# Kernel optimization log

Hardware: AMD Instinct MI355X
Metric: run time of the kernel (lower is better)

## Reference

```python
import jax, jax.numpy as jnp
import numpy as np

B, T, D, H = 4, 2048, 1024, 16
HD = D // H  # head_dim = 64


def _make_freqs():
    # standard RoPE angles: theta_i = 10000^{-2i/hd}
    inv_freq = 1.0 / (10000.0 ** (np.arange(0, HD, 2, dtype=np.float32) / HD))  # [HD/2]
    angles = np.arange(T, dtype=np.float32)[:, None] * inv_freq[None, :]        # [T, HD/2]
    return jnp.asarray(np.cos(angles)), jnp.asarray(np.sin(angles))


def setup_inputs() -> dict:
    key = jax.random.key(0)
    ks = jax.random.split(key, 5)
    freqs_cos, freqs_sin = _make_freqs()
    s = 1.0 / np.sqrt(D)
    return {
        "q": jax.random.normal(ks[0], (B, T, D), jnp.float32),
        "freqs_cos": freqs_cos,
        "freqs_sin": freqs_sin,
        "qkv_w": jax.random.normal(ks[1], (3 * D, D), jnp.float32) * s,
        "qkv_b": jax.random.normal(ks[2], (3 * D,), jnp.float32) * 0.01,
        "o_w": jax.random.normal(ks[3], (D, D), jnp.float32) * s,
        "o_b": jax.random.normal(ks[4], (D,), jnp.float32) * 0.01,
    }


def _apply_rope(x, cos, sin):
    # x: [B, T, H, HD]; cos/sin: [T, HD/2]
    xr = x.reshape(*x.shape[:-1], HD // 2, 2)
    x0, x1 = xr[..., 0], xr[..., 1]
    c = cos[None, :, None, :]
    s = sin[None, :, None, :]
    o0 = x0 * c - x1 * s
    o1 = x0 * s + x1 * c
    return jnp.stack([o0, o1], axis=-1).reshape(x.shape)


def reference(q, freqs_cos, freqs_sin, qkv_w, qkv_b, o_w, o_b):
    # fused QKV projection (torch Linear: x @ W.T + b)
    qkv = q @ qkv_w.T + qkv_b                      # [B, T, 3D]
    qh, kh, vh = jnp.split(qkv, 3, axis=-1)
    qh = qh.reshape(B, T, H, HD)
    kh = kh.reshape(B, T, H, HD)
    vh = vh.reshape(B, T, H, HD)
    qh = _apply_rope(qh, freqs_cos, freqs_sin)
    kh = _apply_rope(kh, freqs_cos, freqs_sin)
    # scaled dot-product attention, no mask, no dropout (eval)
    scale = 1.0 / np.sqrt(HD)
    scores = jnp.einsum('bqhd,bkhd->bhqk', qh, kh) * scale
    probs = jax.nn.softmax(scores, axis=-1)
    out = jnp.einsum('bhqk,bkhd->bqhd', probs, vh).reshape(B, T, D)
    return out @ o_w.T + o_b
```

## Files before the change

### kernel.cpp

```cpp
#include <hip/hip_runtime.h>

#define B_  4
#define T_  2048
#define D_  1024
#define H_  16
#define HD_ 64
#define M_  8192
#define N1_ 3072
#define K_  1024

typedef __bf16 bf16x8 __attribute__((ext_vector_type(8)));
typedef float  f32x4  __attribute__((ext_vector_type(4)));
typedef float  f32x16 __attribute__((ext_vector_type(16)));

__device__ __forceinline__ unsigned short f2bf(float f) {
  union { float f; unsigned u; } v; v.f = f;
  unsigned u = v.u;
  unsigned r = (u + 0x7fffu + ((u >> 16) & 1u)) >> 16;
  return (unsigned short)r;
}
__device__ __forceinline__ float bf2f(unsigned short h) {
  union { unsigned u; float f; } v; v.u = ((unsigned)h) << 16;
  return v.f;
}
__device__ __forceinline__ unsigned pk2(float a, float b) {
  union { __bf16 h[2]; unsigned u; } t;
  t.h[0] = (__bf16)a; t.h[1] = (__bf16)b;
  return t.u;
}
__device__ __forceinline__ void plswap(unsigned &a, unsigned &b) {
  asm("v_permlane32_swap_b32 %0, %1" : "+v"(a), "+v"(b));
}
__device__ __forceinline__ float fexp2(float x) {
  float r;
  asm("v_exp_f32 %0, %1" : "=v"(r) : "v"(x));
  return r;
}

__device__ __forceinline__ void gl_lds16(const unsigned short* g, unsigned short* l) {
  __builtin_amdgcn_global_load_lds(
      (const __attribute__((address_space(1))) unsigned int*)g,
      (__attribute__((address_space(3))) unsigned int*)l,
      16, 0, 0);
}

#define NQ4  ((M_*K_)/4)
#define NW14 ((N1_*K_)/4)
#define NW24 ((D_*K_)/4)
__global__ void cvt_all(const float* __restrict__ q, const float* __restrict__ w1,
                        const float* __restrict__ w2,
                        unsigned short* __restrict__ qo, unsigned short* __restrict__ w1o,
                        unsigned short* __restrict__ w2o) {
  int i = blockIdx.x * 256 + threadIdx.x;
  const float* in; unsigned short* out; int idx;
  if (i < NQ4)              { in = q;  out = qo;  idx = i; }
  else if (i < NQ4 + NW14)  { in = w1; out = w1o; idx = i - NQ4; }
  else if (i < NQ4 + NW14 + NW24) { in = w2; out = w2o; idx = i - NQ4 - NW14; }
  else return;
  float4 f = ((const float4*)in)[idx];
  ushort4 o;
  o.x = f2bf(f.x); o.y = f2bf(f.y); o.z = f2bf(f.z); o.w = f2bf(f.w);
  ((ushort4*)out)[idx] = o;
}

__global__ __launch_bounds__(256) void gemm_qkv(
    const unsigned short* __restrict__ A,
    const unsigned short* __restrict__ W,
    const float* __restrict__ bias,
    unsigned short* __restrict__ Qg,
    unsigned short* __restrict__ Kg,
    unsigned short* __restrict__ Vt,
    const float* __restrict__ cosb, const float* __restrict__ sinb)
{
  __shared__ unsigned short As[128*64];
  __shared__ unsigned short Bs[128*64];
  const int tid = threadIdx.x;
  const int lane = tid & 63, wave = tid >> 6;
  const int wr = wave >> 1, wc = wave & 1;
  const int lr = lane & 15, lg = lane >> 4;
  const int sw = lr & 7;
  const long m0 = (long)blockIdx.x * 128;
  const int  n0 = blockIdx.y * 128;

  f32x4 acc[4][4];
#pragma unroll
  for (int i = 0; i < 4; ++i)
#pragma unroll
    for (int j = 0; j < 4; ++j) acc[i][j] = (f32x4){0.f,0.f,0.f,0.f};

  for (int kt = 0; kt < K_/64; ++kt) {
    __syncthreads();
#pragma unroll
    for (int p = 0; p < 4; ++p) {
      int slot = p*256 + tid;
      int row = slot >> 3, sc = slot & 7, ch = sc ^ (row & 7);
      gl_lds16(A + (m0 + row)*K_ + kt*64 + ch*8, &As[slot*8]);
      gl_lds16(W + ((long)n0 + row)*K_ + kt*64 + ch*8, &Bs[slot*8]);
    }
    __syncthreads();
#pragma unroll
    for (int kk = 0; kk < 2; ++kk) {
      bf16x8 af[4], bfr[4];
#pragma unroll
      for (int i = 0; i < 4; ++i) {
        af[i]  = *(const bf16x8*)&As[(wr*64 + i*16 + lr)*64 + (((lg + 4*kk) ^ sw) * 8)];
        bfr[i] = *(const bf16x8*)&Bs[(wc*64 + i*16 + lr)*64 + (((lg + 4*kk) ^ sw) * 8)];
      }
#pragma unroll
      for (int i = 0; i < 4; ++i)
#pragma unroll
        for (int j = 0; j < 4; ++j)
          acc[i][j] = __builtin_amdgcn_mfma_f32_16x16x32_bf16(af[i], bfr[j], acc[i][j], 0, 0, 0);
    }
  }

#pragma unroll
  for (int j = 0; j < 4; ++j) {
    int n = n0 + wc*64 + j*16 + lr;
    float bv = bias[n];
    int part = n >> 10;
    int d = n & 1023;
    int h = d >> 6, hd = d & 63;
    if (part == 2) {
#pragma unroll
      for (int i = 0; i < 4; ++i) {
        long m = m0 + wr*64 + i*16 + lg*4;
        int b = (int)(m >> 11), t = (int)(m & 2047);
        ushort4 st;
        st.x = f2bf(acc[i][j][0] + bv);
        st.y = f2bf(acc[i][j][1] + bv);
        st.z = f2bf(acc[i][j][2] + bv);
        st.w = f2bf(acc[i][j][3] + bv);
        *(ushort4*)(Vt + ((long)((b*H_ + h)*HD_ + hd))*T_ + t) = st;
      }
    } else if (part == 0) {
#pragma unroll
      for (int i = 0; i < 4; ++i) {
#pragma unroll
        for (int r = 0; r < 4; ++r) {
          long m = m0 + wr*64 + i*16 + lg*4 + r;
          int b = (int)(m >> 11), t = (int)(m & 2047);
          Qg[(((long)(b*H_ + h))*T_ + t)*HD_ + hd] = f2bf(acc[i][j][r] + bv);
        }
      }
    } else {
      const int u   = hd >> 1;
      const int odd = lr & 1;
#pragma unroll
      for (int i = 0; i < 4; ++i) {
#pragma unroll
        for (int r = 0; r < 4; ++r) {
          long m = m0 + wr*64 + i*16 + lg*4 + r;
          int b = (int)(m >> 11), t = (int)(m & 2047);
          float v = acc[i][j][r] + bv;
          float p = __shfl_xor(v, 1);
          float cu = cosb[t*32 + u], su = sinb[t*32 + u];
          float res = odd ? (p*su + v*cu) : (v*cu - p*su);
          Kg[(((long)(b*H_ + h))*T_ + t)*HD_ + hd] = f2bf(res);
        }
      }
    }
  }
}

__global__ __launch_bounds__(256) void flash_attn(
    const unsigned short* __restrict__ Qg, const unsigned short* __restrict__ Kg,
    const unsigned short* __restrict__ Vt, unsigned short* __restrict__ attn,
    const float* __restrict__ cosb, const float* __restrict__ sinb)
{
  __shared__ unsigned short Ks0[64*64], Vs0[64*64];
  __shared__ unsigned short Ks1[64*64], Vs1[64*64];
  const int tid = threadIdx.x, lane = tid & 63, wave = tid >> 6;
  const int lq = lane & 31, hi = lane >> 5;
  const int id = blockIdx.x;
  const int bh = (id & 7)*8 + ((id >> 3) & 7);
  const int q0 = (id >> 6)*128 + wave*32;
  const long kvbase = (long)bh * T_ * HD_;
  const int fsw = (lq & 7) ^ (lq >> 3);

  bf16x8 qf[4];
  {
    const int tq = q0 + lq;
    const unsigned short* qrow = Qg + kvbase + (long)tq*HD_;
    const float* crow = cosb + tq*32;
    const float* srow = sinb + tq*32;
    const float scl = 0.125f * 1.44269504f;
#pragma unroll
    for (int c = 0; c < 4; ++c) {
      bf16x8 raw = *(const bf16x8*)(qrow + c*16 + hi*8);
      const unsigned short* e = (const unsigned short*)&raw;
      bf16x8 outv;
#pragma unroll
      for (int j = 0; j < 4; ++j) {
        float x0 = bf2f(e[2*j]), x1 = bf2f(e[2*j+1]);
        float cv = crow[c*8 + hi*4 + j], sv = srow[c*8 + hi*4 + j];
        outv[2*j]   = (__bf16)((x0*cv - x1*sv) * scl);
        outv[2*j+1] = (__bf16)((x0*sv + x1*cv) * scl);
      }
      qf[c] = outv;
    }
  }

  f32x16 oA, oB;
#pragma unroll
  for (int r = 0; r < 16; ++r) { oA[r] = 0.f; oB[r] = 0.f; }
  float l = 0.f;

  const int slotA = tid, slotB = 256 + tid;
  const int rwA = slotA >> 3, rwB = slotB >> 3;
  const int chA = (slotA & 7) ^ ((rwA & 7) ^ ((rwA >> 3) & 7));
  const int chB = (slotB & 7) ^ ((rwB & 7) ^ ((rwB >> 3) & 7));
  const unsigned short* KsrcA = Kg + kvbase + (long)rwA*HD_ + chA*8;
  const unsigned short* KsrcB = Kg + kvbase + (long)rwB*HD_ + chB*8;
  const unsigned short* VsrcA = Vt + (long)(bh*HD_ + rwA)*T_ + chA*8;
  const unsigned short* VsrcB = Vt + (long)(bh*HD_ + rwB)*T_ + chB*8;

#define STAGE0(kt) {                                      \
    gl_lds16(KsrcA + (kt)*64*HD_, &Ks0[slotA*8]);         \
    gl_lds16(KsrcB + (kt)*64*HD_, &Ks0[slotB*8]);         \
    gl_lds16(VsrcA + (kt)*64,     &Vs0[slotA*8]);         \
    gl_lds16(VsrcB + (kt)*64,     &Vs0[slotB*8]);         \
  }
#define STAGE1(kt) {                                      \
    gl_lds16(KsrcA + (kt)*64*HD_, &Ks1[slotA*8]);         \
    gl_lds16(KsrcB + (kt)*64*HD_, &Ks1[slotB*8]);         \
    gl_lds16(VsrcA + (kt)*64,     &Vs1[slotA*8]);         \
    gl_lds16(VsrcB + (kt)*64,     &Vs1[slotB*8]);         \
  }

#define FBODY(KSB, VSB)                                                                   \
  _Pragma("unroll")                                                                       \
  for (int kf = 0; kf < 2; ++kf) {                                                        \
    bf16x8 ka[4];                                                                         \
    _Pragma("unroll")                                                                     \
    for (int c = 0; c < 4; ++c)                                                           \
      ka[c] = *(const bf16x8*)&KSB[(kf*32 + lq)*64 + (((2*c + hi) ^ fsw ^ (kf*4)) * 8)];  \
    f32x16 cf;                                                                            \
    _Pragma("unroll")                                                                     \
    for (int r = 0; r < 16; ++r) cf[r] = 0.f;                                             \
    __builtin_amdgcn_s_setprio(1);                                                        \
    cf = __builtin_amdgcn_mfma_f32_32x32x16_bf16(ka[0], qf[0], cf, 0, 0, 0);              \
    cf = __builtin_amdgcn_mfma_f32_32x32x16_bf16(ka[1], qf[1], cf, 0, 0, 0);              \
    cf = __builtin_amdgcn_mfma_f32_32x32x16_bf16(ka[2], qf[2], cf, 0, 0, 0);              \
    cf = __builtin_amdgcn_mfma_f32_32x32x16_bf16(ka[3], qf[3], cf, 0, 0, 0);              \
    __builtin_amdgcn_s_setprio(0);                                                        \
    float p[16];                                                                          \
    _Pragma("unroll")                                                                     \
    for (int r = 0; r < 16; ++r) p[r] = fexp2(cf[r]);                                     \
    {                                                                                     \
      float s01 = (p[0]+p[1]) + (p[2]+p[3]);                                              \
      float s23 = (p[4]+p[5]) + (p[6]+p[7]);                                              \
      float s45 = (p[8]+p[9]) + (p[10]+p[11]);                                            \
      float s67 = (p[12]+p[13]) + (p[14]+p[15]);                                          \
      l += (s01 + s23) + (s45 + s67);                                                     \
    }                                                                                     \
    unsigned qx0 = pk2(p[0],  p[1]),  qy0 = pk2(p[2],  p[3]);                             \
    unsigned qx1 = pk2(p[4],  p[5]),  qy1 = pk2(p[6],  p[7]);                             \
    unsigned qx2 = pk2(p[8],  p[9]),  qy2 = pk2(p[10], p[11]);                            \
    unsigned qx3 = pk2(p[12], p[13]), qy3 = pk2(p[14], p[15]);                            \
    plswap(qx0, qx1); plswap(qy0, qy1);                                                   \
    plswap(qx2, qx3); plswap(qy2, qy3);                                                   \
    union { unsigned w[4]; bf16x8 v; } u0, u1;                                            \
    u0.w[0] = qx0; u0.w[1] = qy0; u0.w[2] = qx1; u0.w[3] = qy1;                           \
    u1.w[0] = qx2; u1.w[1] = qy2; u1.w[2] = qx3; u1.w[3] = qy3;                           \
    bf16x8 pf0 = u0.v, pf1 = u1.v;                                                        \
    bf16x8 va00 = *(const bf16x8*)&VSB[(lq)*64      + (((4*kf + 0 + hi) ^ fsw) * 8)];     \
    bf16x8 va01 = *(const bf16x8*)&VSB[(lq)*64      + (((4*kf + 2 + hi) ^ fsw) * 8)];     \
    bf16x8 va10 = *(const bf16x8*)&VSB[(32 + lq)*64 + (((4*kf + 0 + hi) ^ fsw ^ 4) * 8)]; \
    bf16x8 va11 = *(const bf16x8*)&VSB[(32 + lq)*64 + (((4*kf + 2 + hi) ^ fsw ^ 4) * 8)]; \
    __builtin_amdgcn_s_setprio(1);                                                        \
    oA = __builtin_amdgcn_mfma_f32_32x32x16_bf16(va00, pf0, oA, 0, 0, 0);                 \
    oA = __builtin_amdgcn_mfma_f32_32x32x16_bf16(va01, pf1, oA, 0, 0, 0);                 \
    oB = __builtin_amdgcn_mfma_f32_32x32x16_bf16(va10, pf0, oB, 0, 0, 0);                 \
    oB = __builtin_amdgcn_mfma_f32_32x32x16_bf16(va11, pf1, oB, 0, 0, 0);                 \
    __builtin_amdgcn_s_setprio(0);                                                        \
  }

  STAGE0(0);
  __syncthreads();

  for (int kt = 0; kt < T_/64; kt += 2) {
    STAGE1(kt + 1);
    FBODY(Ks0, Vs0);
    __syncthreads();
    if (kt + 2 < T_/64) STAGE0(kt + 2);
    FBODY(Ks1, Vs1);
    __syncthreads();
  }
#undef STAGE0
#undef STAGE1
#undef FBODY

  l += __shfl_xor(l, 32);
  int b = bh >> 4, h = bh & 15;
  float inv = 1.0f / l;
  long rowb = ((long)(b*T_ + q0 + lq))*D_ + h*HD_;
#pragma unroll
  for (int g = 0; g < 4; ++g) {
    ushort4 st;
    st.x = f2bf(oA[4*g+0] * inv);
    st.y = f2bf(oA[4*g+1] * inv);
    st.z = f2bf(oA[4*g+2] * inv);
    st.w = f2bf(oA[4*g+3] * inv);
    *(ushort4*)(attn + rowb + 8*g + 4*hi) = st;
  }
#pragma unroll
  for (int g = 0; g < 4; ++g) {
    ushort4 st;
    st.x = f2bf(oB[4*g+0] * inv);
    st.y = f2bf(oB[4*g+1] * inv);
    st.z = f2bf(oB[4*g+2] * inv);
    st.w = f2bf(oB[4*g+3] * inv);
    *(ushort4*)(attn + rowb + 32 + 8*g + 4*hi) = st;
  }
}

__global__ __launch_bounds__(256) void gemm_out(
    const unsigned short* __restrict__ A,
    const unsigned short* __restrict__ W,
    const float* __restrict__ bias,
    float* __restrict__ C)
{
  __shared__ unsigned short As[128*64];
  __shared__ unsigned short Bs[128*64];
  const int tid = threadIdx.x;
  const int lane = tid & 63, wave = tid >> 6;
  const int wr = wave >> 1, wc = wave & 1;
  const int lr = lane & 15, lg = lane >> 4;
  const int sw = lr & 7;
  const long m0 = (long)blockIdx.x * 128;
  const int  n0 = blockIdx.y * 128;

  f32x4 acc[4][4];
#pragma unroll
  for (int i = 0; i < 4; ++i)
#pragma unroll
    for (int j = 0; j < 4; ++j) acc[i][j] = (f32x4){0.f,0.f,0.f,0.f};

  for (int kt = 0; kt < K_/64; ++kt) {
    __syncthreads();
#pragma unroll
    for (int p = 0; p < 4; ++p) {
      int slot = p*256 + tid;
      int row = slot >> 3, sc = slot & 7, ch = sc ^ (row & 7);
      gl_lds16(A + (m0 + row)*K_ + kt*64 + ch*8, &As[slot*8]);
      gl_lds16(W + ((long)n0 + row)*K_ + kt*64 + ch*8, &Bs[slot*8]);
    }
    __syncthreads();
#pragma unroll
    for (int kk = 0; kk < 2; ++kk) {
      bf16x8 af[4], bfr[4];
#pragma unroll
      for (int i = 0; i < 4; ++i) {
        af[i]  = *(const bf16x8*)&As[(wr*64 + i*16 + lr)*64 + (((lg + 4*kk) ^ sw) * 8)];
        bfr[i] = *(const bf16x8*)&Bs[(wc*64 + i*16 + lr)*64 + (((lg + 4*kk) ^ sw) * 8)];
      }
#pragma unroll
      for (int i = 0; i < 4; ++i)
#pragma unroll
        for (int j = 0; j < 4; ++j)
          acc[i][j] = __builtin_amdgcn_mfma_f32_16x16x32_bf16(af[i], bfr[j], acc[i][j], 0, 0, 0);
    }
  }

#pragma unroll
  for (int j = 0; j < 4; ++j) {
    int n = n0 + wc*64 + j*16 + lr;
    float bv = bias[n];
#pragma unroll
    for (int i = 0; i < 4; ++i) {
#pragma unroll
      for (int r = 0; r < 4; ++r) {
        long m = m0 + wr*64 + i*16 + lg*4 + r;
        C[m*D_ + n] = acc[i][j][r] + bv;
      }
    }
  }
}

extern "C" void kernel_launch(void* const* d_in, const int* in_sizes, int n_in,
                              void* d_out, int out_size, void* d_ws, size_t ws_size,
                              hipStream_t stream)
{
  const float* q     = (const float*)d_in[0];
  const float* fcos  = (const float*)d_in[1];
  const float* fsin  = (const float*)d_in[2];
  const float* qkv_w = (const float*)d_in[3];
  const float* qkv_b = (const float*)d_in[4];
  const float* o_w   = (const float*)d_in[5];
  const float* o_b   = (const float*)d_in[6];
  float* out = (float*)d_out;

  char* ws = (char*)d_ws;
  unsigned short* qbf  = (unsigned short*)(ws);
  unsigned short* w1bf = (unsigned short*)(ws + 16777216);
  unsigned short* w2bf = (unsigned short*)(ws + 16777216 + 6291456);
  unsigned short* Qg   = (unsigned short*)(ws + 25165824);
  unsigned short* Kg   = (unsigned short*)(ws + 41943040);
  unsigned short* Vt   = (unsigned short*)(ws + 58720256);

  int ncvt = NQ4 + NW14 + NW24;
  cvt_all<<<(ncvt + 255)/256, 256, 0, stream>>>(q, qkv_w, o_w, qbf, w1bf, w2bf);

  dim3 g1(M_/128, N1_/128);
  gemm_qkv<<<g1, 256, 0, stream>>>(qbf, w1bf, qkv_b, Qg, Kg, Vt, fcos, fsin);

  unsigned short* attn = qbf;
  flash_attn<<<1024, 256, 0, stream>>>(Qg, Kg, Vt, attn, fcos, fsin);

  dim3 g2(M_/128, D_/128);
  gemm_out<<<g2, 256, 0, stream>>>(attn, w2bf, o_b, out);
}
```

Measured before the change: 203.8 us.

## Use four-buffer K/V ring with prefetch distance two and vmcnt waits

The attention kernel's K/V staging moves from a double buffer with two __syncthreads per pair of tiles to a four-slot LDS ring. Loads are issued two tiles ahead, and each step uses a single s_waitcnt vmcnt(8) plus a barrier, so the kernel waits only for the tile it is about to use. This aims to hide global-to-LDS latency more deeply and cut barrier overhead. In exchange, LDS per block doubles to 64 KB, which can lower the number of resident blocks per CU. The hand-written vmcnt counts also assume the exact load ordering the compiler emits.

```diff
diff --git a/kernel.cpp b/kernel.cpp
--- a/kernel.cpp
+++ b/kernel.cpp
@@ -170,6 +170,8 @@
 {
   __shared__ unsigned short Ks0[64*64], Vs0[64*64];
   __shared__ unsigned short Ks1[64*64], Vs1[64*64];
+  __shared__ unsigned short Ks2[64*64], Vs2[64*64];
+  __shared__ unsigned short Ks3[64*64], Vs3[64*64];
   const int tid = threadIdx.x, lane = tid & 63, wave = tid >> 6;
   const int lq = lane & 31, hi = lane >> 5;
   const int id = blockIdx.x;
@@ -215,18 +217,22 @@
   const unsigned short* VsrcA = Vt + (long)(bh*HD_ + rwA)*T_ + chA*8;
   const unsigned short* VsrcB = Vt + (long)(bh*HD_ + rwB)*T_ + chB*8;
 
-#define STAGE0(kt) {                                      \
-    gl_lds16(KsrcA + (kt)*64*HD_, &Ks0[slotA*8]);         \
-    gl_lds16(KsrcB + (kt)*64*HD_, &Ks0[slotB*8]);         \
-    gl_lds16(VsrcA + (kt)*64,     &Vs0[slotA*8]);         \
-    gl_lds16(VsrcB + (kt)*64,     &Vs0[slotB*8]);         \
-  }
-#define STAGE1(kt) {                                      \
-    gl_lds16(KsrcA + (kt)*64*HD_, &Ks1[slotA*8]);         \
-    gl_lds16(KsrcB + (kt)*64*HD_, &Ks1[slotB*8]);         \
-    gl_lds16(VsrcA + (kt)*64,     &Vs1[slotA*8]);         \
-    gl_lds16(VsrcB + (kt)*64,     &Vs1[slotB*8]);         \
-  }
+#define STG(kt, KSB, VSB) {                               \
+    gl_lds16(KsrcA + (kt)*64*HD_, &KSB[slotA*8]);         \
+    gl_lds16(KsrcB + (kt)*64*HD_, &KSB[slotB*8]);         \
+    gl_lds16(VsrcA + (kt)*64,     &VSB[slotA*8]);         \
+    gl_lds16(VsrcB + (kt)*64,     &VSB[slotB*8]);         \
+  }
+
+#define WB8 { asm volatile("s_waitcnt vmcnt(8) lgkmcnt(0)" ::: "memory");  \
+              __builtin_amdgcn_s_barrier();                                \
+              __builtin_amdgcn_sched_barrier(0); }
+#define WB4 { asm volatile("s_waitcnt vmcnt(4) lgkmcnt(0)" ::: "memory");  \
+              __builtin_amdgcn_s_barrier();                                \
+              __builtin_amdgcn_sched_barrier(0); }
+#define WB0 { asm volatile("s_waitcnt vmcnt(0) lgkmcnt(0)" ::: "memory");  \
+              __builtin_amdgcn_s_barrier();                                \
+              __builtin_amdgcn_sched_barrier(0); }
 
 #define FBODY(KSB, VSB)                                                                   \
   _Pragma("unroll")                                                                       \
@@ -276,19 +282,23 @@
     __builtin_amdgcn_s_setprio(0);                                                        \
   }
 
-  STAGE0(0);
-  __syncthreads();
-
-  for (int kt = 0; kt < T_/64; kt += 2) {
-    STAGE1(kt + 1);
-    FBODY(Ks0, Vs0);
-    __syncthreads();
-    if (kt + 2 < T_/64) STAGE0(kt + 2);
-    FBODY(Ks1, Vs1);
-    __syncthreads();
-  }
-#undef STAGE0
-#undef STAGE1
+  STG(0, Ks0, Vs0);
+  STG(1, Ks1, Vs1);
+
+  for (int kt = 0; kt <= 24; kt += 4) {
+    STG(kt + 2, Ks2, Vs2);  WB8;  FBODY(Ks0, Vs0);
+    STG(kt + 3, Ks3, Vs3);  WB8;  FBODY(Ks1, Vs1);
+    STG(kt + 4, Ks0, Vs0);  WB8;  FBODY(Ks2, Vs2);
+    STG(kt + 5, Ks1, Vs1);  WB8;  FBODY(Ks3, Vs3);
+  }
+  STG(30, Ks2, Vs2);  WB8;  FBODY(Ks0, Vs0);
+  STG(31, Ks3, Vs3);  WB8;  FBODY(Ks1, Vs1);
+  WB4;  FBODY(Ks2, Vs2);
+  WB0;  FBODY(Ks3, Vs3);
+#undef STG
+#undef WB8
+#undef WB4
+#undef WB0
 #undef FBODY
 
   l += __shfl_xor(l, 32);
```

After: 206.2 us. No clear change (+1.2%).
